# Performance work log

Hardware: AMD Instinct MI355X
Metric: run time of the kernel (lower is better)

Reference implementation:

```python
import jax, jax.numpy as jnp
import numpy as np

N = 32768      # total nodes (2048 graphs * 16 nodes)
E = 491520     # total edges (2048 graphs * 16*15)
F = 11         # in_node_nf
H = 64         # hidden_nf
G = 2048       # number of graphs
NN = 16        # nodes per graph
R = 1024       # n_reactions
L = 4          # n_layers
EIN = 2 * H + 1        # edge_mlp input: [h[row], h[col], radial]
NIN = H + H + F        # node_mlp input: [h, agg, node_attr=h0]


def setup_inputs() -> dict:
    key = jax.random.key(0)
    ks = jax.random.split(key, 24)
    s = 0.05
    d = {
        "h0": jax.random.normal(ks[0], (N, F), jnp.float32),
        "positions": jax.random.normal(ks[1], (N, 3), jnp.float32),
        "edges": jax.random.randint(ks[2], (2, E), 0, N),
        "node_mask": jnp.ones((N, 1), jnp.float32),
        "edge_mask": jnp.ones((E, 1), jnp.float32),
        "reaction_indexes": jax.random.randint(ks[3], (G,), 0, R),
        "reaction_signs": jax.random.normal(ks[4], (G,), jnp.float32),
        # params
        "emb_w": jax.random.normal(ks[5], (F, H), jnp.float32) * s,
        "emb_b": jnp.zeros((H,), jnp.float32),
        "edge_w1": jax.random.normal(ks[6], (L, EIN, H), jnp.float32) * s,
        "edge_b1": jnp.zeros((L, H), jnp.float32),
        "edge_w2": jax.random.normal(ks[7], (L, H, H), jnp.float32) * s,
        "edge_b2": jnp.zeros((L, H), jnp.float32),
        "node_w1": jax.random.normal(ks[8], (L, NIN, H), jnp.float32) * s,
        "node_b1": jnp.zeros((L, H), jnp.float32),
        "node_w2": jax.random.normal(ks[9], (L, H, H), jnp.float32) * s,
        "node_b2": jnp.zeros((L, H), jnp.float32),
        "dec_w1": jax.random.normal(ks[10], (H, H), jnp.float32) * s,
        "dec_b1": jnp.zeros((H,), jnp.float32),
        "dec_w2": jax.random.normal(ks[11], (H, H), jnp.float32) * s,
        "dec_b2": jnp.zeros((H,), jnp.float32),
        "g_w1": jax.random.normal(ks[12], (H, H), jnp.float32) * s,
        "g_b1": jnp.zeros((H,), jnp.float32),
        "g_w2": jax.random.normal(ks[13], (H, 1), jnp.float32) * s,
        "g_b2": jnp.zeros((1,), jnp.float32),
        "n_nodes": NN,
        "n_reactions": R,
    }
    return d


def reference(h0, positions, edges, node_mask, edge_mask, reaction_indexes,
              reaction_signs, emb_w, emb_b, edge_w1, edge_b1, edge_w2, edge_b2,
              node_w1, node_b1, node_w2, node_b2, dec_w1, dec_b1, dec_w2,
              dec_b2, g_w1, g_b1, g_w2, g_b2, n_nodes, n_reactions):
    silu = jax.nn.silu
    row, col = edges[0], edges[1]
    n = h0.shape[0]

    # radial is constant across layers (coords never updated in this variant)
    coord_diff = positions[row] - positions[col]          # [E, 3]
    radial = jnp.sum(coord_diff ** 2, axis=1, keepdims=True)  # [E, 1]

    h = h0 @ emb_w + emb_b                                # [N, H]
    for i in range(edge_w1.shape[0]):
        # edge model
        e_in = jnp.concatenate([h[row], h[col], radial], axis=1)  # [E, 2H+1]
        e = silu(e_in @ edge_w1[i] + edge_b1[i])
        e = silu(e @ edge_w2[i] + edge_b2[i])             # [E, H]
        e = e * edge_mask
        # scatter-sum aggregation by source node
        agg = jax.ops.segment_sum(e, row, num_segments=n)  # [N, H]
        # node model (node_attr = h0)
        n_in = jnp.concatenate([h, agg, h0], axis=1)      # [N, 2H+F]
        h = silu(n_in @ node_w1[i] + node_b1[i]) @ node_w2[i] + node_b2[i]

    # node decoder
    h = silu(h @ dec_w1 + dec_b1) @ dec_w2 + dec_b2
    h = h * node_mask
    # pool per graph (fixed n_nodes per graph)
    hg = h.reshape(-1, n_nodes, h.shape[-1]).sum(axis=1)  # [G, H]
    # graph decoder
    temp = silu(hg @ g_w1 + g_b1) @ g_w2 + g_b2           # [G, 1]
    # signed per-reaction aggregation
    pred = jnp.zeros((n_reactions,), h.dtype).at[reaction_indexes].add(
        temp[:, 0] * reaction_signs)
    return pred
```

## Files before the change

### kernel.cpp

```cpp
#include <hip/hip_runtime.h>
#include <math.h>
#include <stdint.h>

#define N_NODES 32768
#define N_EDGES 491520
#define F_IN    11
#define H       64
#define G_GRAPHS 2048
#define NN_PER_G 16
#define R_REACT 1024
#define L_LAYERS 4
#define EIN     129
#define NIN     139
#define NPBLK   32

#define WPROJ 0
#define WE2   65536
#define WN1   98304
#define WN2   180224
#define WD1   212992
#define WD2   221184
#define WTOT  229376

typedef __attribute__((ext_vector_type(8))) short short8;
// ... 38 lines not shown

    if (b < 64) {
        int l = b >> 4, f = b & 15;
        int nt = f >> 1, kf = f & 1;
#pragma unroll
        for (int j = 0; j < 8; ++j) {
            int row = (nt >= 4 ? 64 : 0) + kf * 32 + quad * 8 + j;
            unsigned short hi, lo;
            splitbf(ew1[l * EIN * H + row * H + (nt & 3) * 16 + m16], hi, lo);
            h8[j] = (short)hi; l8[j] = (short)lo;
        }
        base = wsW + WPROJ + l * 16384; fidx = f; half = 8192;
    } else if (b < 96) {
        int bb = b - 64; int l = bb >> 3, f = bb & 7;
        int nt = f >> 1, kf = f & 1;
#pragma unroll
        for (int j = 0; j < 8; ++j) {
            int row = kf * 32 + quad * 8 + j;
            unsigned short hi, lo;
            splitbf(ew2[l * H * H + row * H + nt * 16 + m16], hi, lo);
            h8[j] = (short)hi; l8[j] = (short)lo;
        }
        base = wsW + WE2 + l * 8192; fidx = f; half = 4096;
    } else if (b < 176) {
        int bb = b - 96; int l = bb / 20, f = bb % 20;
        int nt = f / 5, kf = f % 5;
#pragma unroll
        for (int j = 0; j < 8; ++j) {
            int row = kf * 32 + quad * 8 + j;
            float w = (row < NIN) ? nw1[l * NIN * H + row * H + nt * 16 + m16] : 0.0f;
            unsigned short hi, lo; splitbf(w, hi, lo);
            h8[j] = (short)hi; l8[j] = (short)lo;
        }
        base = wsW + WN1 + l * 20480; fidx = f; half = 10240;
    } else if (b < 208) {
        int bb = b - 176; int l = bb >> 3, f = bb & 7;
        int nt = f >> 1, kf = f & 1;
#pragma unroll
        for (int j = 0; j < 8; ++j) {
            int row = kf * 32 + quad * 8 + j;
            unsigned short hi, lo;
            splitbf(nw2[l * H * H + row * H + nt * 16 + m16], hi, lo);
            h8[j] = (short)hi; l8[j] = (short)lo;
        }
        base = wsW + WN2 + l * 8192; fidx = f; half = 4096;
    } else if (b < 216) {
        int f = b - 208;
        int nt = f >> 1, kf = f & 1;
#pragma unroll
        for (int j = 0; j < 8; ++j) {
            int row = kf * 32 + quad * 8 + j;
            unsigned short hi, lo;
            splitbf(dw1[row * H + nt * 16 + m16], hi, lo);
            h8[j] = (short)hi; l8[j] = (short)lo;
        }
        base = wsW + WD1; fidx = f; half = 4096;
    } else {
        int f = b - 216;
        int nt = f >> 1, kf = f & 1;
#pragma unroll
        for (int j = 0; j < 8; ++j) {
            int row = kf * 32 + quad * 8 + j;
            unsigned short hi, lo;
            splitbf(dw2[row * H + nt * 16 + m16], hi, lo);
            h8[j] = (short)hi; l8[j] = (short)lo;
        }
        base = wsW + WD2; fidx = f; half = 4096;
    }
    *(short8*)(base + (fidx * 64 + lane) * 8) = h8;
    *(short8*)(base + half + (fidx * 64 + lane) * 8) = l8;
}

__global__ __launch_bounds__(256) void k_embed(
        const float* __restrict__ h0, const float* __restrict__ emb_w,
        const float* __restrict__ emb_b, float* __restrict__ h) {
    int tid = blockIdx.x * 256 + threadIdx.x;
    int n = tid >> 6, j = tid & 63;
    float acc = emb_b[j];
#pragma unroll
    for (int k = 0; k < F_IN; ++k)
        acc += h0[n * F_IN + k] * emb_w[k * H + j];
    h[tid] = acc;
}

__global__ __launch_bounds__(256) void k_radial(
        const int* __restrict__ edges, const float* __restrict__ pos,
        float* __restrict__ radial) {
    int e = blockIdx.x * 256 + threadIdx.x;
    int r = edges[e], c = edges[N_EDGES + e];
    float dx = pos[r * 3 + 0] - pos[c * 3 + 0];
    float dy = pos[r * 3 + 1] - pos[c * 3 + 1];
    float dz = pos[r * 3 + 2] - pos[c * 3 + 2];
    radial[e] = dx * dx + dy * dy + dz * dz;
}

__global__ __launch_bounds__(256) void k_hist(
        const int* __restrict__ edges, int* __restrict__ deg) {
    int e = blockIdx.x * 256 + threadIdx.x;
    atomicAdd(&deg[edges[e]], 1);
}

__global__ __launch_bounds__(128) void k_scan_blk(
        const int* __restrict__ deg, int* __restrict__ off,
        int* __restrict__ bsum) {
    __shared__ int sd[128];
    int b = blockIdx.x;
    sd[threadIdx.x] = deg[b * 128 + threadIdx.x];
    __syncthreads();
    if (threadIdx.x == 0) {
        int s = 0;
        for (int i = 0; i < 128; ++i) { int d = sd[i]; sd[i] = s; s += d; }
        bsum[b] = s;
    }
    __syncthreads();
    off[b * 128 + threadIdx.x] = sd[threadIdx.x];
}

__global__ __launch_bounds__(256) void k_scan_top(
        const int* __restrict__ bsum, int* __restrict__ bbase) {
    __shared__ int sb[256];
    sb[threadIdx.x] = bsum[threadIdx.x];
    __syncthreads();
    if (threadIdx.x == 0) {
        int s = 0;
        for (int i = 0; i < 256; ++i) { int d = sb[i]; sb[i] = s; s += d; }
    }
    __syncthreads();
    bbase[threadIdx.x] = sb[threadIdx.x];
}

__global__ __launch_bounds__(256) void k_cursor(
        const int* __restrict__ off, const int* __restrict__ bbase,
        int* __restrict__ nstart, int* __restrict__ cursor) {
    int n = blockIdx.x * 256 + threadIdx.x;
    int ns = off[n] + bbase[n >> 7];
    nstart[n] = ns;
    cursor[n] = ns;
    if (n == 0) nstart[N_NODES] = N_EDGES;
}

__global__ __launch_bounds__(256) void k_fill(
        const int* __restrict__ edges, const float* __restrict__ radial,
        const float* __restrict__ emask, int* __restrict__ cursor,
        int* __restrict__ csrP, float* __restrict__ csrR,
        float* __restrict__ csrM) {
    int e = blockIdx.x * 256 + threadIdx.x;
    int r = edges[e];
    int pos = atomicAdd(&cursor[r], 1);
    csrP[pos] = edges[N_EDGES + e] | ((r & (NPBLK - 1)) << 16);
    csrR[pos] = radial[e];
    csrM[pos] = emask[e];
}

__global__ __launch_bounds__(64, 1) void k_nodeproj_m(
        const float* __restrict__ h, const short* __restrict__ wP,
        const float* __restrict__ b1,
        float* __restrict__ PA, float* __restrict__ PB) {
    const int lane = threadIdx.x;
    const int quad = lane >> 4, m16 = lane & 15;

    short8 Bh[16], Bl[16];
#pragma unroll
    for (int f = 0; f < 16; ++f) {
        Bh[f] = *(const short8*)(wP + (f * 64 + lane) * 8);
        Bl[f] = *(const short8*)(wP + 8192 + (f * 64 + lane) * 8);
    }
    float b1v[4];
#pragma unroll
    for (int nt = 0; nt < 4; ++nt) b1v[nt] = b1[nt * 16 + m16];

    for (int t = 0; t < 2; ++t) {
        const int nb = (blockIdx.x * 2 + t) * 16;
        const float* hp = h + (nb + m16) * H + quad * 8;
        float av[16];
        *(float4*)&av[0]  = *(const float4*)(hp + 0);
        *(float4*)&av[4]  = *(const float4*)(hp + 4);
        *(float4*)&av[8]  = *(const float4*)(hp + 32);
        *(float4*)&av[12] = *(const float4*)(hp + 36);
        short8 Ah0, Ah1, Al0, Al1;
#pragma unroll
        for (int j = 0; j < 8; ++j) {
            unsigned short hi, lo;
            splitbf_t(av[j], hi, lo);     Ah0[j] = (short)hi; Al0[j] = (short)lo;
            splitbf_t(av[8 + j], hi, lo); Ah1[j] = (short)hi; Al1[j] = (short)lo;
        }
        f32x4 acc[8];
#pragma unroll
        for (int nt = 0; nt < 8; ++nt) {
            f32x4 a = {0.0f, 0.0f, 0.0f, 0.0f};
            a = __builtin_amdgcn_mfma_f32_16x16x32_bf16(Ah0, Bh[nt*2+0], a, 0, 0, 0);
            a = __builtin_amdgcn_mfma_f32_16x16x32_bf16(Ah1, Bh[nt*2+1], a, 0, 0, 0);
            a = __builtin_amdgcn_mfma_f32_16x16x32_bf16(Ah0, Bl[nt*2+0], a, 0, 0, 0);
            a = __builtin_amdgcn_mfma_f32_16x16x32_bf16(Ah1, Bl[nt*2+1], a, 0, 0, 0);
            a = __builtin_amdgcn_mfma_f32_16x16x32_bf16(Al0, Bh[nt*2+0], a, 0, 0, 0);
            a = __builtin_amdgcn_mfma_f32_16x16x32_bf16(Al1, Bh[nt*2+1], a, 0, 0, 0);
            acc[nt] = a;
        }
#pragma unroll
        for (int r4 = 0; r4 < 4; ++r4) {
            const int node = nb + quad * 4 + r4;
#pragma unroll
            for (int nt = 0; nt < 4; ++nt)
                PA[node * H + nt * 16 + m16] = acc[nt][r4] + b1v[nt];
#pragma unroll
            for (int nt = 4; nt < 8; ++nt)
                PB[node * H + (nt - 4) * 16 + m16] = acc[nt][r4];
        }
    }
}

__global__ __launch_bounds__(256, 2) void k_edge6(
        const float* __restrict__ PA, const float* __restrict__ PB,
        const int* __restrict__ nstart, const int* __restrict__ csrP,
        const float* __restrict__ csrR, const float* __restrict__ csrM,
        const float* __restrict__ W1,
        const short* __restrict__ wE2, const float* __restrict__ b2,
        float* __restrict__ agg) {
    const int tid = threadIdx.x;
    const int lane = tid & 63, wave = tid >> 6;
    const int quad = lane >> 4, m16 = lane & 15;
    const int n0 = blockIdx.x * NPBLK;

    __shared__ float aggld[NPBLK * 68];
    __shared__ short blds[8 * 64 * 8];
    for (int i = tid; i < NPBLK * 68; i += 256) aggld[i] = 0.0f;
    for (int i = tid; i < 8 * 64; i += 256)
        *(short8*)(blds + i * 8) = *(const short8*)(wE2 + 4096 + i * 8);

    short8 Bh[8];
#pragma unroll
    for (int f = 0; f < 8; ++f)
        Bh[f] = *(const short8*)(wE2 + (f * 64 + lane) * 8);
    float w1cr[16];
#pragma unroll
    for (int i = 0; i < 16; ++i) {
        int k = (i < 8) ? (quad * 8 + i) : (32 + quad * 8 + (i - 8));
        w1cr[i] = W1[128 * H + k];
    }
    float b2v[4];
#pragma unroll
    for (int nt = 0; nt < 4; ++nt) b2v[nt] = b2[nt * 16 + m16];

    const int start = nstart[n0];
    const int end   = nstart[n0 + NPBLK];
    __syncthreads();

    const int ntiles = (end - start + 15) >> 4;

    int   pkA = 0, pkB = 0;
    float radA = 0.0f, radB = 0.0f, mkA = 0.0f, mkB = 0.0f;
    float avA[16], bvA[16];

    int tA = wave;
    bool haveA = tA < ntiles;
    if (haveA) {
        const int idx = start + tA * 16 + m16;
        const int ss  = min(idx, N_EDGES - 1);
        pkA  = csrP[ss];
        radA = csrR[ss];
        mkA  = (idx < end) ? csrM[ss] : 0.0f;
        const int c  = pkA & 0xFFFF;
        const int rl = pkA >> 16;
        const float* par = PA + (n0 + rl) * H + quad * 8;
        const float* pbr = PB + c * H + quad * 8;
        *(float4*)&avA[0]  = *(const float4*)(par + 0);
        *(float4*)&avA[4]  = *(const float4*)(par + 4);
        *(float4*)&avA[8]  = *(const float4*)(par + 32);
        *(float4*)&avA[12] = *(const float4*)(par + 36);
        *(float4*)&bvA[0]  = *(const float4*)(pbr + 0);
        *(float4*)&bvA[4]  = *(const float4*)(pbr + 4);
        *(float4*)&bvA[8]  = *(const float4*)(pbr + 32);
        *(float4*)&bvA[12] = *(const float4*)(pbr + 36);
    }
    int tB = tA + 4;
    bool haveB = tB < ntiles;
    if (haveB) {
        const int idx = start + tB * 16 + m16;
        const int ss  = min(idx, N_EDGES - 1);
        pkB  = csrP[ss];
        radB = csrR[ss];
        mkB  = (idx < end) ? csrM[ss] : 0.0f;
    }

    while (haveA) {
        float bvB[16];
        if (haveB) {
            const int c = pkB & 0xFFFF;
            const float* pbr = PB + c * H + quad * 8;
            *(float4*)&bvB[0]  = *(const float4*)(pbr + 0);
            *(float4*)&bvB[4]  = *(const float4*)(pbr + 4);
            *(float4*)&bvB[8]  = *(const float4*)(pbr + 32);
            *(float4*)&bvB[12] = *(const float4*)(pbr + 36);
        }
        const int tC = tB + 4;
        const bool haveC = tC < ntiles;
        int pkC = 0; float radC = 0.0f, mkC = 0.0f;
        if (haveC) {
            const int idx = start + tC * 16 + m16;
            const int ss  = min(idx, N_EDGES - 1);
            pkC  = csrP[ss];
            radC = csrR[ss];
            mkC  = (idx < end) ? csrM[ss] : 0.0f;
        }

        short8 Ah0, Ah1, Al0, Al1;
#pragma unroll
        for (int i = 0; i < 8; ++i) {
            unsigned short hi, lo;
            splitbf_t(silu_f(avA[i] + bvA[i] + radA * w1cr[i]), hi, lo);
            Ah0[i] = (short)hi; Al0[i] = (short)lo;
            splitbf_t(silu_f(avA[8+i] + bvA[8+i] + radA * w1cr[8+i]), hi, lo);
            Ah1[i] = (short)hi; Al1[i] = (short)lo;
        }
        f32x4 acc[4];
#pragma unroll
        for (int nt = 0; nt < 4; ++nt) {
            f32x4 a = {0.0f, 0.0f, 0.0f, 0.0f};
            a = __builtin_amdgcn_mfma_f32_16x16x32_bf16(Ah0, Bh[nt*2+0], a, 0, 0, 0);
            a = __builtin_amdgcn_mfma_f32_16x16x32_bf16(Ah1, Bh[nt*2+1], a, 0, 0, 0);
            short8 bl0 = *(const short8*)(blds + ((nt*2+0) * 64 + lane) * 8);
            short8 bl1 = *(const short8*)(blds + ((nt*2+1) * 64 + lane) * 8);
            a = __builtin_amdgcn_mfma_f32_16x16x32_bf16(Ah0, bl0, a, 0, 0, 0);
            a = __builtin_amdgcn_mfma_f32_16x16x32_bf16(Ah1, bl1, a, 0, 0, 0);
            a = __builtin_amdgcn_mfma_f32_16x16x32_bf16(Al0, Bh[nt*2+0], a, 0, 0, 0);
            a = __builtin_amdgcn_mfma_f32_16x16x32_bf16(Al1, Bh[nt*2+1], a, 0, 0, 0);
            acc[nt] = a;
        }

        int rlq[4]; float mkq[4];
#pragma unroll
        for (int r4 = 0; r4 < 4; ++r4) {
            rlq[r4] = __shfl(pkA, quad * 4 + r4) >> 16;
            mkq[r4] = __shfl(mkA, quad * 4 + r4);
        }
#pragma unroll
        for (int nt = 0; nt < 4; ++nt) {
            float oo[4];
#pragma unroll
            for (int r4 = 0; r4 < 4; ++r4)
                oo[r4] = silu_f(acc[nt][r4] + b2v[nt]) * mkq[r4];
            int cur = rlq[0]; float s = oo[0];
#pragma unroll
            for (int r4 = 1; r4 < 4; ++r4) {
                if (rlq[r4] == cur) { s += oo[r4]; }
                else {
                    atomicAdd(&aggld[cur * 68 + nt * 16 + m16], s);
                    cur = rlq[r4]; s = oo[r4];
                }
            }
            atomicAdd(&aggld[cur * 68 + nt * 16 + m16], s);
        }

        if (haveB) {
            const int rl = pkB >> 16;
            const float* par = PA + (n0 + rl) * H + quad * 8;
            *(float4*)&avA[0]  = *(const float4*)(par + 0);
            *(float4*)&avA[4]  = *(const float4*)(par + 4);
            *(float4*)&avA[8]  = *(const float4*)(par + 32);
            *(float4*)&avA[12] = *(const float4*)(par + 36);
#pragma unroll
            for (int i = 0; i < 16; ++i) bvA[i] = bvB[i];
            pkA = pkB; radA = radB; mkA = mkB;
        }
        pkB = pkC; radB = radC; mkB = mkC;
        tB = tC; haveA = haveB; haveB = haveC;
    }

    __syncthreads();
#pragma unroll
    for (int i = tid; i < NPBLK * 16; i += 256) {
        int n = i >> 4, cb = (i & 15) << 2;
        *(float4*)&agg[(n0 + n) * H + cb] = *(const float4*)&aggld[n * 68 + cb];
    }
}

__global__ __launch_bounds__(64, 1) void k_node_m(
        float* __restrict__ h, const float* __restrict__ agg,
        const float* __restrict__ h0,
        const short* __restrict__ wN1, const float* __restrict__ b1,
        const short* __restrict__ wN2, const float* __restrict__ b2) {
    const int lane = threadIdx.x;
    const int quad = lane >> 4, m16 = lane & 15;

    short8 B1h[20], B1l[20];
#pragma unroll
    for (int f = 0; f < 20; ++f) {
        B1h[f] = *(const short8*)(wN1 + (f * 64 + lane) * 8);
        B1l[f] = *(const short8*)(wN1 + 10240 + (f * 64 + lane) * 8);
    }
    short8 B2h[8], B2l[8];
#pragma unroll
    for (int f = 0; f < 8; ++f) {
        B2h[f] = *(const short8*)(wN2 + (f * 64 + lane) * 8);
        B2l[f] = *(const short8*)(wN2 + 4096 + (f * 64 + lane) * 8);
    }
    float b1v[4], b2v[4];
#pragma unroll
    for (int nt = 0; nt < 4; ++nt) {
        b1v[nt] = b1[nt * 16 + m16];
        b2v[nt] = b2[nt * 16 + m16];
    }

    __shared__ float tld[16 * 68];

    for (int t = 0; t < 2; ++t) {
        const int nb = (blockIdx.x * 2 + t) * 16;
        float a1[5][8];
        const float* hp = h + (nb + m16) * H + quad * 8;
        const float* ap = agg + (nb + m16) * H + quad * 8;
        *(float4*)&a1[0][0] = *(const float4*)(hp + 0);
        *(float4*)&a1[0][4] = *(const float4*)(hp + 4);
        *(float4*)&a1[1][0] = *(const float4*)(hp + 32);
        *(float4*)&a1[1][4] = *(const float4*)(hp + 36);
        *(float4*)&a1[2][0] = *(const float4*)(ap + 0);
        *(float4*)&a1[2][4] = *(const float4*)(ap + 4);
        *(float4*)&a1[3][0] = *(const float4*)(ap + 32);
        *(float4*)&a1[3][4] = *(const float4*)(ap + 36);
        const float* h0p = h0 + (nb + m16) * F_IN;
#pragma unroll
        for (int j = 0; j < 8; ++j) {
            int kk = quad * 8 + j;
            a1[4][j] = (kk < F_IN) ? h0p[kk] : 0.0f;
        }
        short8 A1h[5], A1l[5];
#pragma unroll
        for (int kf = 0; kf < 5; ++kf) {
            short8 ah, al;
#pragma unroll
            for (int j = 0; j < 8; ++j) {
                unsigned short hi, lo; splitbf_t(a1[kf][j], hi, lo);
                ah[j] = (short)hi; al[j] = (short)lo;
            }
            A1h[kf] = ah; A1l[kf] = al;
        }
        f32x4 acc[4];
#pragma unroll
        for (int nt = 0; nt < 4; ++nt) {
            f32x4 a = {0.0f, 0.0f, 0.0f, 0.0f};
#pragma unroll
            for (int kf = 0; kf < 5; ++kf)
                a = __builtin_amdgcn_mfma_f32_16x16x32_bf16(A1h[kf], B1h[nt*5+kf], a, 0, 0, 0);
#pragma unroll
            for (int kf = 0; kf < 5; ++kf)
                a = __builtin_amdgcn_mfma_f32_16x16x32_bf16(A1h[kf], B1l[nt*5+kf], a, 0, 0, 0);
#pragma unroll
            for (int kf = 0; kf < 5; ++kf)
                a = __builtin_amdgcn_mfma_f32_16x16x32_bf16(A1l[kf], B1h[nt*5+kf], a, 0, 0, 0);
            acc[nt] = a;
        }
#pragma unroll
        for (int r4 = 0; r4 < 4; ++r4)
#pragma unroll
            for (int nt = 0; nt < 4; ++nt)
                tld[(quad * 4 + r4) * 68 + nt * 16 + m16] =
                    silu_f(acc[nt][r4] + b1v[nt]);
        __syncthreads();
        float a2[16];
        *(float4*)&a2[0]  = *(const float4*)&tld[m16 * 68 + quad * 8 + 0];
        *(float4*)&a2[4]  = *(const float4*)&tld[m16 * 68 + quad * 8 + 4];
        *(float4*)&a2[8]  = *(const float4*)&tld[m16 * 68 + quad * 8 + 32];
        *(float4*)&a2[12] = *(const float4*)&tld[m16 * 68 + quad * 8 + 36];
        short8 A2h0, A2h1, A2l0, A2l1;
#pragma unroll
        for (int j = 0; j < 8; ++j) {
            unsigned short hi, lo;
            splitbf_t(a2[j], hi, lo);     A2h0[j] = (short)hi; A2l0[j] = (short)lo;
            splitbf_t(a2[8+j], hi, lo);   A2h1[j] = (short)hi; A2l1[j] = (short)lo;
        }
        f32x4 acc2[4];
#pragma unroll
        for (int nt = 0; nt < 4; ++nt) {
            f32x4 a = {0.0f, 0.0f, 0.0f, 0.0f};
            a = __builtin_amdgcn_mfma_f32_16x16x32_bf16(A2h0, B2h[nt*2+0], a, 0, 0, 0);
            a = __builtin_amdgcn_mfma_f32_16x16x32_bf16(A2h1, B2h[nt*2+1], a, 0, 0, 0);
            a = __builtin_amdgcn_mfma_f32_16x16x32_bf16(A2h0, B2l[nt*2+0], a, 0, 0, 0);
            a = __builtin_amdgcn_mfma_f32_16x16x32_bf16(A2h1, B2l[nt*2+1], a, 0, 0, 0);
            a = __builtin_amdgcn_mfma_f32_16x16x32_bf16(A2l0, B2h[nt*2+0], a, 0, 0, 0);
            a = __builtin_amdgcn_mfma_f32_16x16x32_bf16(A2l1, B2h[nt*2+1], a, 0, 0, 0);
            acc2[nt] = a;
        }
#pragma unroll
        for (int r4 = 0; r4 < 4; ++r4) {
            const int node = nb + quad * 4 + r4;
#pragma unroll
            for (int nt = 0; nt < 4; ++nt)
                h[node * H + nt * 16 + m16] = acc2[nt][r4] + b2v[nt];
        }
        __syncthreads();
    }
}

__global__ __launch_bounds__(64, 1) void k_dec_m(
        float* __restrict__ h, const float* __restrict__ nmask,
        const short* __restrict__ wD1, const float* __restrict__ b1,
        const short* __restrict__ wD2, const float* __restrict__ b2) {
    const int lane = threadIdx.x;
    const int quad = lane >> 4, m16 = lane & 15;

    short8 B1h[8], B1l[8], B2h[8], B2l[8];
#pragma unroll
    for (int f = 0; f < 8; ++f) {
        B1h[f] = *(const short8*)(wD1 + (f * 64 + lane) * 8);
        B1l[f] = *(const short8*)(wD1 + 4096 + (f * 64 + lane) * 8);
        B2h[f] = *(const short8*)(wD2 + (f * 64 + lane) * 8);
        B2l[f] = *(const short8*)(wD2 + 4096 + (f * 64 + lane) * 8);
    }
    float b1v[4], b2v[4];
#pragma unroll
    for (int nt = 0; nt < 4; ++nt) {
        b1v[nt] = b1[nt * 16 + m16];
        b2v[nt] = b2[nt * 16 + m16];
    }
    __shared__ float tld[16 * 68];

    for (int t = 0; t < 2; ++t) {
        const int nb = (blockIdx.x * 2 + t) * 16;
        const float* hp = h + (nb + m16) * H + quad * 8;
        float av[16];
        *(float4*)&av[0]  = *(const float4*)(hp + 0);
        *(float4*)&av[4]  = *(const float4*)(hp + 4);
        *(float4*)&av[8]  = *(const float4*)(hp + 32);
        *(float4*)&av[12] = *(const float4*)(hp + 36);
        short8 Ah0, Ah1, Al0, Al1;
#pragma unroll
        for (int j = 0; j < 8; ++j) {
            unsigned short hi, lo;
            splitbf_t(av[j], hi, lo);     Ah0[j] = (short)hi; Al0[j] = (short)lo;
            splitbf_t(av[8+j], hi, lo);   Ah1[j] = (short)hi; Al1[j] = (short)lo;
        }
        f32x4 acc[4];
#pragma unroll
        for (int nt = 0; nt < 4; ++nt) {
            f32x4 a = {0.0f, 0.0f, 0.0f, 0.0f};
            a = __builtin_amdgcn_mfma_f32_16x16x32_bf16(Ah0, B1h[nt*2+0], a, 0, 0, 0);
            a = __builtin_amdgcn_mfma_f32_16x16x32_bf16(Ah1, B1h[nt*2+1], a, 0, 0, 0);
            a = __builtin_amdgcn_mfma_f32_16x16x32_bf16(Ah0, B1l[nt*2+0], a, 0, 0, 0);
            a = __builtin_amdgcn_mfma_f32_16x16x32_bf16(Ah1, B1l[nt*2+1], a, 0, 0, 0);
            a = __builtin_amdgcn_mfma_f32_16x16x32_bf16(Al0, B1h[nt*2+0], a, 0, 0, 0);
            a = __builtin_amdgcn_mfma_f32_16x16x32_bf16(Al1, B1h[nt*2+1], a, 0, 0, 0);
            acc[nt] = a;
        }
#pragma unroll
        for (int r4 = 0; r4 < 4; ++r4)
#pragma unroll
            for (int nt = 0; nt < 4; ++nt)
                tld[(quad * 4 + r4) * 68 + nt * 16 + m16] =
                    silu_f(acc[nt][r4] + b1v[nt]);
        __syncthreads();
        float a2[16];
        *(float4*)&a2[0]  = *(const float4*)&tld[m16 * 68 + quad * 8 + 0];
        *(float4*)&a2[4]  = *(const float4*)&tld[m16 * 68 + quad * 8 + 4];
        *(float4*)&a2[8]  = *(const float4*)&tld[m16 * 68 + quad * 8 + 32];
        *(float4*)&a2[12] = *(const float4*)&tld[m16 * 68 + quad * 8 + 36];
        short8 A2h0, A2h1, A2l0, A2l1;
#pragma unroll
        for (int j = 0; j < 8; ++j) {
            unsigned short hi, lo;
            splitbf_t(a2[j], hi, lo);     A2h0[j] = (short)hi; A2l0[j] = (short)lo;
            splitbf_t(a2[8+j], hi, lo);   A2h1[j] = (short)hi; A2l1[j] = (short)lo;
        }
        f32x4 acc2[4];
#pragma unroll
        for (int nt = 0; nt < 4; ++nt) {
            f32x4 a = {0.0f, 0.0f, 0.0f, 0.0f};
            a = __builtin_amdgcn_mfma_f32_16x16x32_bf16(A2h0, B2h[nt*2+0], a, 0, 0, 0);
            a = __builtin_amdgcn_mfma_f32_16x16x32_bf16(A2h1, B2h[nt*2+1], a, 0, 0, 0);
            a = __builtin_amdgcn_mfma_f32_16x16x32_bf16(A2h0, B2l[nt*2+0], a, 0, 0, 0);
            a = __builtin_amdgcn_mfma_f32_16x16x32_bf16(A2h1, B2l[nt*2+1], a, 0, 0, 0);
            a = __builtin_amdgcn_mfma_f32_16x16x32_bf16(A2l0, B2h[nt*2+0], a, 0, 0, 0);
            a = __builtin_amdgcn_mfma_f32_16x16x32_bf16(A2l1, B2h[nt*2+1], a, 0, 0, 0);
            acc2[nt] = a;
        }
#pragma unroll
        for (int r4 = 0; r4 < 4; ++r4) {
            const int node = nb + quad * 4 + r4;
            const float nm = nmask[node];
#pragma unroll
            for (int nt = 0; nt < 4; ++nt)
                h[node * H + nt * 16 + m16] = (acc2[nt][r4] + b2v[nt]) * nm;
        }
        __syncthreads();
    }
}

__global__ __launch_bounds__(64) void k_graph(
        const float* __restrict__ h, const int* __restrict__ rid,
        const float* __restrict__ rsign,
        const float* __restrict__ W1, const float* __restrict__ b1,
        const float* __restrict__ W2, const float* __restrict__ b2,
        float* __restrict__ pred) {
    const int g = blockIdx.x;
    const int lane = threadIdx.x;
    float hgv = 0.0f;
#pragma unroll
    for (int m = 0; m < NN_PER_G; ++m)
        hgv += h[(g * NN_PER_G + m) * H + lane];
    __shared__ __align__(16) float hgs[64];
    hgs[lane] = hgv;
    __syncthreads();
    float acc = b1[lane];
#pragma unroll
    for (int k = 0; k < H; ++k)
        acc += hgs[k] * W1[k * H + lane];
    float part = silu_f(acc) * W2[lane];
#pragma unroll
    for (int off = 32; off > 0; off >>= 1)
        part += __shfl_down(part, off);
    if (lane == 0)
        atomAddF(&pred[rid[g]], (part + b2[0]) * rsign[g]);
}

extern "C" void kernel_launch(void* const* d_in, const int* in_sizes, int n_in,
                              void* d_out, int out_size, void* d_ws, size_t ws_size,
                              hipStream_t stream) {
    const float* h0      = (const float*)d_in[0];
    const float* pos     = (const float*)d_in[1];
    const int*   edges   = (const int*)d_in[2];
    const float* nmask   = (const float*)d_in[3];
    const float* emask   = (const float*)d_in[4];
    const int*   rid     = (const int*)d_in[5];
    const float* rsign   = (const float*)d_in[6];
    const float* emb_w   = (const float*)d_in[7];
    const float* emb_b   = (const float*)d_in[8];
    const float* edge_w1 = (const float*)d_in[9];
    const float* edge_b1 = (const float*)d_in[10];
    const float* edge_w2 = (const float*)d_in[11];
    const float* edge_b2 = (const float*)d_in[12];
    const float* node_w1 = (const float*)d_in[13];
    const float* node_b1 = (const float*)d_in[14];
    const float* node_w2 = (const float*)d_in[15];
    const float* node_b2 = (const float*)d_in[16];
    const float* dec_w1  = (const float*)d_in[17];
    const float* dec_b1  = (const float*)d_in[18];
    const float* dec_w2  = (const float*)d_in[19];
    const float* dec_b2  = (const float*)d_in[20];
    const float* g_w1    = (const float*)d_in[21];
    const float* g_b1    = (const float*)d_in[22];
    const float* g_w2    = (const float*)d_in[23];
    const float* g_b2    = (const float*)d_in[24];

    float* h      = (float*)d_ws;
    float* agg    = h + N_NODES * H;
    float* radial = agg + N_NODES * H;
    float* PA     = radial + N_EDGES;
    float* PB     = PA + N_NODES * H;
    float* csrR   = PB + N_NODES * H;
    float* csrM   = csrR + N_EDGES;
    int*   csrP   = (int*)(csrM + N_EDGES);
    int*   deg    = csrP + N_EDGES;
    int*   off    = deg + N_NODES;
    int*   bsum   = off + N_NODES;
    int*   bbase  = bsum + 256;
    int*   nstart = bbase + 256;
    int*   cursor = nstart + N_NODES + 1;
    short* wsW    = (short*)((((uintptr_t)(cursor + N_NODES)) + 255) & ~(uintptr_t)255);
    float* pred   = (float*)d_out;

    hipMemsetAsync(d_out, 0, R_REACT * sizeof(float), stream);
    hipMemsetAsync(deg, 0, N_NODES * sizeof(int), stream);

    k_prepw<<<224, 64, 0, stream>>>(edge_w1, edge_w2, node_w1, node_w2,
                                    dec_w1, dec_w2, wsW);
    k_embed<<<(N_NODES * H) / 256, 256, 0, stream>>>(h0, emb_w, emb_b, h);
    k_radial<<<N_EDGES / 256, 256, 0, stream>>>(edges, pos, radial);
    k_hist<<<N_EDGES / 256, 256, 0, stream>>>(edges, deg);
    k_scan_blk<<<256, 128, 0, stream>>>(deg, off, bsum);
    k_scan_top<<<1, 256, 0, stream>>>(bsum, bbase);
    k_cursor<<<N_NODES / 256, 256, 0, stream>>>(off, bbase, nstart, cursor);
    k_fill<<<N_EDGES / 256, 256, 0, stream>>>(edges, radial, emask, cursor,
                                              csrP, csrR, csrM);

    for (int i = 0; i < L_LAYERS; ++i) {
        k_nodeproj_m<<<N_NODES / 32, 64, 0, stream>>>(
            h, wsW + WPROJ + i * 16384, edge_b1 + i * H, PA, PB);
        k_edge6<<<N_NODES / NPBLK, 256, 0, stream>>>(
            PA, PB, nstart, csrP, csrR, csrM,
            edge_w1 + i * EIN * H,
            wsW + WE2 + i * 8192, edge_b2 + i * H, agg);
        k_node_m<<<N_NODES / 32, 64, 0, stream>>>(
            h, agg, h0,
            wsW + WN1 + i * 20480, node_b1 + i * H,
            wsW + WN2 + i * 8192,  node_b2 + i * H);
    }
    k_dec_m<<<N_NODES / 32, 64, 0, stream>>>(h, nmask, wsW + WD1, dec_b1,
                                             wsW + WD2, dec_b2);
    k_graph<<<G_GRAPHS, 64, 0, stream>>>(h, rid, rsign, g_w1, g_b1, g_w2,
                                         g_b2, pred);
}
```

Measured before the change: 563.6 us.

## Stream weights per tile in node kernels and hold edge weights in registers

The node projection, node MLP and decoder kernels stop preloading every weight fragment into registers. They now handle one 16-node tile per block, reload the weights inside the output-column loop, and launch twice as many blocks with a higher occupancy hint. The edge kernel moves the low-half second-layer weights from LDS into registers. It also reads the row-local index and mask per quad straight from the CSR arrays instead of using shuffles, and it fixes the tA tile rotation. Register pressure and block size go down in exchange for more repeated global or L2 weight loads, and the edge kernel uses more registers.

```diff
diff --git a/kernel.cpp b/kernel.cpp
--- a/kernel.cpp
+++ b/kernel.cpp
@@ -214,59 +214,51 @@
     csrM[pos] = emask[e];
 }
 
-__global__ __launch_bounds__(64, 1) void k_nodeproj_m(
+__global__ __launch_bounds__(64, 2) void k_nodeproj_m(
         const float* __restrict__ h, const short* __restrict__ wP,
         const float* __restrict__ b1,
         float* __restrict__ PA, float* __restrict__ PB) {
     const int lane = threadIdx.x;
     const int quad = lane >> 4, m16 = lane & 15;
-
-    short8 Bh[16], Bl[16];
-#pragma unroll
-    for (int f = 0; f < 16; ++f) {
-        Bh[f] = *(const short8*)(wP + (f * 64 + lane) * 8);
-        Bl[f] = *(const short8*)(wP + 8192 + (f * 64 + lane) * 8);
-    }
+    const int nb = blockIdx.x * 16;
+
+    const float* hp = h + (nb + m16) * H + quad * 8;
+    float av[16];
+    *(float4*)&av[0]  = *(const float4*)(hp + 0);
+    *(float4*)&av[4]  = *(const float4*)(hp + 4);
+    *(float4*)&av[8]  = *(const float4*)(hp + 32);
+    *(float4*)&av[12] = *(const float4*)(hp + 36);
     float b1v[4];
 #pragma unroll
     for (int nt = 0; nt < 4; ++nt) b1v[nt] = b1[nt * 16 + m16];
 
-    for (int t = 0; t < 2; ++t) {
-        const int nb = (blockIdx.x * 2 + t) * 16;
-        const float* hp = h + (nb + m16) * H + quad * 8;
-        float av[16];
-        *(float4*)&av[0]  = *(const float4*)(hp + 0);
-        *(float4*)&av[4]  = *(const float4*)(hp + 4);
-        *(float4*)&av[8]  = *(const float4*)(hp + 32);
-        *(float4*)&av[12] = *(const float4*)(hp + 36);
-        short8 Ah0, Ah1, Al0, Al1;
-#pragma unroll
-        for (int j = 0; j < 8; ++j) {
-            unsigned short hi, lo;
-            splitbf_t(av[j], hi, lo);     Ah0[j] = (short)hi; Al0[j] = (short)lo;
-            splitbf_t(av[8 + j], hi, lo); Ah1[j] = (short)hi; Al1[j] = (short)lo;
-        }
-        f32x4 acc[8];
-#pragma unroll
-        for (int nt = 0; nt < 8; ++nt) {
-            f32x4 a = {0.0f, 0.0f, 0.0f, 0.0f};
-            a = __builtin_amdgcn_mfma_f32_16x16x32_bf16(Ah0, Bh[nt*2+0], a, 0, 0, 0);
-            a = __builtin_amdgcn_mfma_f32_16x16x32_bf16(Ah1, Bh[nt*2+1], a, 0, 0, 0);
-            a = __builtin_amdgcn_mfma_f32_16x16x32_bf16(Ah0, Bl[nt*2+0], a, 0, 0, 0);
-            a = __builtin_amdgcn_mfma_f32_16x16x32_bf16(Ah1, Bl[nt*2+1], a, 0, 0, 0);
-            a = __builtin_amdgcn_mfma_f32_16x16x32_bf16(Al0, Bh[nt*2+0], a, 0, 0, 0);
-            a = __builtin_amdgcn_mfma_f32_16x16x32_bf16(Al1, Bh[nt*2+1], a, 0, 0, 0);
-            acc[nt] = a;
-        }
+    short8 Ah0, Ah1, Al0, Al1;
+#pragma unroll
+    for (int j = 0; j < 8; ++j) {
+        unsigned short hi, lo;
+        splitbf_t(av[j], hi, lo);     Ah0[j] = (short)hi; Al0[j] = (short)lo;
+        splitbf_t(av[8 + j], hi, lo); Ah1[j] = (short)hi; Al1[j] = (short)lo;
+    }
+#pragma unroll
+    for (int nt = 0; nt < 8; ++nt) {
+        short8 bh0 = *(const short8*)(wP + ((nt*2+0) * 64 + lane) * 8);
+        short8 bh1 = *(const short8*)(wP + ((nt*2+1) * 64 + lane) * 8);
+        short8 bl0 = *(const short8*)(wP + 8192 + ((nt*2+0) * 64 + lane) * 8);
+        short8 bl1 = *(const short8*)(wP + 8192 + ((nt*2+1) * 64 + lane) * 8);
+        f32x4 a = {0.0f, 0.0f, 0.0f, 0.0f};
+        a = __builtin_amdgcn_mfma_f32_16x16x32_bf16(Ah0, bh0, a, 0, 0, 0);
+        a = __builtin_amdgcn_mfma_f32_16x16x32_bf16(Ah1, bh1, a, 0, 0, 0);
+        a = __builtin_amdgcn_mfma_f32_16x16x32_bf16(Ah0, bl0, a, 0, 0, 0);
+        a = __builtin_amdgcn_mfma_f32_16x16x32_bf16(Ah1, bl1, a, 0, 0, 0);
+        a = __builtin_amdgcn_mfma_f32_16x16x32_bf16(Al0, bh0, a, 0, 0, 0);
+        a = __builtin_amdgcn_mfma_f32_16x16x32_bf16(Al1, bh1, a, 0, 0, 0);
 #pragma unroll
         for (int r4 = 0; r4 < 4; ++r4) {
             const int node = nb + quad * 4 + r4;
-#pragma unroll
-            for (int nt = 0; nt < 4; ++nt)
-                PA[node * H + nt * 16 + m16] = acc[nt][r4] + b1v[nt];
-#pragma unroll
-            for (int nt = 4; nt < 8; ++nt)
-                PB[node * H + (nt - 4) * 16 + m16] = acc[nt][r4];
+            if (nt < 4)
+                PA[node * H + nt * 16 + m16] = a[r4] + b1v[nt];
+            else
+                PB[node * H + (nt - 4) * 16 + m16] = a[r4];
         }
     }
 }
@@ -284,15 +276,14 @@
     const int n0 = blockIdx.x * NPBLK;
 
     __shared__ float aggld[NPBLK * 68];
-    __shared__ short blds[8 * 64 * 8];
     for (int i = tid; i < NPBLK * 68; i += 256) aggld[i] = 0.0f;
-    for (int i = tid; i < 8 * 64; i += 256)
-        *(short8*)(blds + i * 8) = *(const short8*)(wE2 + 4096 + i * 8);
-
-    short8 Bh[8];
-#pragma unroll
-    for (int f = 0; f < 8; ++f)
+
+    short8 Bh[8], Bl[8];
+#pragma unroll
+    for (int f = 0; f < 8; ++f) {
         Bh[f] = *(const short8*)(wE2 + (f * 64 + lane) * 8);
+        Bl[f] = *(const short8*)(wE2 + 4096 + (f * 64 + lane) * 8);
+    }
     float w1cr[16];
 #pragma unroll
     for (int i = 0; i < 16; ++i) {
@@ -310,7 +301,7 @@
     const int ntiles = (end - start + 15) >> 4;
 
     int   pkA = 0, pkB = 0;
-    float radA = 0.0f, radB = 0.0f, mkA = 0.0f, mkB = 0.0f;
+    float radA = 0.0f, radB = 0.0f;
     float avA[16], bvA[16];
 
     int tA = wave;
@@ -320,7 +311,6 @@
         const int ss  = min(idx, N_EDGES - 1);
         pkA  = csrP[ss];
         radA = csrR[ss];
-        mkA  = (idx < end) ? csrM[ss] : 0.0f;
         const int c  = pkA & 0xFFFF;
         const int rl = pkA >> 16;
         const float* par = PA + (n0 + rl) * H + quad * 8;
@@ -341,7 +331,6 @@
         const int ss  = min(idx, N_EDGES - 1);
         pkB  = csrP[ss];
         radB = csrR[ss];
-        mkB  = (idx < end) ? csrM[ss] : 0.0f;
     }
 
     while (haveA) {
@@ -356,13 +345,20 @@
         }
         const int tC = tB + 4;
         const bool haveC = tC < ntiles;
-        int pkC = 0; float radC = 0.0f, mkC = 0.0f;
+        int pkC = 0; float radC = 0.0f;
         if (haveC) {
             const int idx = start + tC * 16 + m16;
             const int ss  = min(idx, N_EDGES - 1);
             pkC  = csrP[ss];
             radC = csrR[ss];
-            mkC  = (idx < end) ? csrM[ss] : 0.0f;
+        }
+        int rlq[4]; float mkq[4];
+        const int sb = start + tA * 16 + quad * 4;
+#pragma unroll
+        for (int r4 = 0; r4 < 4; ++r4) {
+            int s = sb + r4, s2 = min(s, N_EDGES - 1);
+            rlq[r4] = csrP[s2] >> 16;
+            mkq[r4] = (s < end) ? csrM[s2] : 0.0f;
         }
 
         short8 Ah0, Ah1, Al0, Al1;
@@ -380,21 +376,13 @@
             f32x4 a = {0.0f, 0.0f, 0.0f, 0.0f};
             a = __builtin_amdgcn_mfma_f32_16x16x32_bf16(Ah0, Bh[nt*2+0], a, 0, 0, 0);
             a = __builtin_amdgcn_mfma_f32_16x16x32_bf16(Ah1, Bh[nt*2+1], a, 0, 0, 0);
-            short8 bl0 = *(const short8*)(blds + ((nt*2+0) * 64 + lane) * 8);
-            short8 bl1 = *(const short8*)(blds + ((nt*2+1) * 64 + lane) * 8);
-            a = __builtin_amdgcn_mfma_f32_16x16x32_bf16(Ah0, bl0, a, 0, 0, 0);
-            a = __builtin_amdgcn_mfma_f32_16x16x32_bf16(Ah1, bl1, a, 0, 0, 0);
+            a = __builtin_amdgcn_mfma_f32_16x16x32_bf16(Ah0, Bl[nt*2+0], a, 0, 0, 0);
+            a = __builtin_amdgcn_mfma_f32_16x16x32_bf16(Ah1, Bl[nt*2+1], a, 0, 0, 0);
             a = __builtin_amdgcn_mfma_f32_16x16x32_bf16(Al0, Bh[nt*2+0], a, 0, 0, 0);
             a = __builtin_amdgcn_mfma_f32_16x16x32_bf16(Al1, Bh[nt*2+1], a, 0, 0, 0);
             acc[nt] = a;
         }
 
-        int rlq[4]; float mkq[4];
-#pragma unroll
-        for (int r4 = 0; r4 < 4; ++r4) {
-            rlq[r4] = __shfl(pkA, quad * 4 + r4) >> 16;
-            mkq[r4] = __shfl(mkA, quad * 4 + r4);
-        }
 #pragma unroll
         for (int nt = 0; nt < 4; ++nt) {
             float oo[4];
@@ -422,10 +410,10 @@
             *(float4*)&avA[12] = *(const float4*)(par + 36);
 #pragma unroll
             for (int i = 0; i < 16; ++i) bvA[i] = bvB[i];
-            pkA = pkB; radA = radB; mkA = mkB;
-        }
-        pkB = pkC; radB = radC; mkB = mkC;
-        tB = tC; haveA = haveB; haveB = haveC;
+            pkA = pkB; radA = radB;
+        }
+        pkB = pkC; radB = radC;
+        tA = tB; tB = tC; haveA = haveB; haveB = haveC;
     }
 
     __syncthreads();
@@ -436,26 +424,15 @@
     }
 }
 
-__global__ __launch_bounds__(64, 1) void k_node_m(
+__global__ __launch_bounds__(64, 2) void k_node_m(
         float* __restrict__ h, const float* __restrict__ agg,
         const float* __restrict__ h0,
         const short* __restrict__ wN1, const float* __restrict__ b1,
         const short* __restrict__ wN2, const float* __restrict__ b2) {
     const int lane = threadIdx.x;
     const int quad = lane >> 4, m16 = lane & 15;
-
-    short8 B1h[20], B1l[20];
-#pragma unroll
-    for (int f = 0; f < 20; ++f) {
-        B1h[f] = *(const short8*)(wN1 + (f * 64 + lane) * 8);
-        B1l[f] = *(const short8*)(wN1 + 10240 + (f * 64 + lane) * 8);
-    }
-    short8 B2h[8], B2l[8];
-#pragma unroll
-    for (int f = 0; f < 8; ++f) {
-        B2h[f] = *(const short8*)(wN2 + (f * 64 + lane) * 8);
-        B2l[f] = *(const short8*)(wN2 + 4096 + (f * 64 + lane) * 8);
-    }
+    const int nb = blockIdx.x * 16;
+
     float b1v[4], b2v[4];
 #pragma unroll
     for (int nt = 0; nt < 4; ++nt) {
@@ -465,108 +442,98 @@
 
     __shared__ float tld[16 * 68];
 
-    for (int t = 0; t < 2; ++t) {
-        const int nb = (blockIdx.x * 2 + t) * 16;
-        float a1[5][8];
-        const float* hp = h + (nb + m16) * H + quad * 8;
-        const float* ap = agg + (nb + m16) * H + quad * 8;
-        *(float4*)&a1[0][0] = *(const float4*)(hp + 0);
-        *(float4*)&a1[0][4] = *(const float4*)(hp + 4);
-        *(float4*)&a1[1][0] = *(const float4*)(hp + 32);
-        *(float4*)&a1[1][4] = *(const float4*)(hp + 36);
-        *(float4*)&a1[2][0] = *(const float4*)(ap + 0);
-        *(float4*)&a1[2][4] = *(const float4*)(ap + 4);
-        *(float4*)&a1[3][0] = *(const float4*)(ap + 32);
-        *(float4*)&a1[3][4] = *(const float4*)(ap + 36);
-        const float* h0p = h0 + (nb + m16) * F_IN;
+    float a1[5][8];
+    const float* hp = h + (nb + m16) * H + quad * 8;
+    const float* ap = agg + (nb + m16) * H + quad * 8;
+    *(float4*)&a1[0][0] = *(const float4*)(hp + 0);
+    *(float4*)&a1[0][4] = *(const float4*)(hp + 4);
+    *(float4*)&a1[1][0] = *(const float4*)(hp + 32);
+    *(float4*)&a1[1][4] = *(const float4*)(hp + 36);
+    *(float4*)&a1[2][0] = *(const float4*)(ap + 0);
+    *(float4*)&a1[2][4] = *(const float4*)(ap + 4);
+    *(float4*)&a1[3][0] = *(const float4*)(ap + 32);
+    *(float4*)&a1[3][4] = *(const float4*)(ap + 36);
+    const float* h0p = h0 + (nb + m16) * F_IN;
+#pragma unroll
+    for (int j = 0; j < 8; ++j) {
+        int kk = quad * 8 + j;
+        a1[4][j] = (kk < F_IN) ? h0p[kk] : 0.0f;
+    }
+    short8 A1h[5], A1l[5];
+#pragma unroll
+    for (int kf = 0; kf < 5; ++kf) {
+        short8 ah, al;
 #pragma unroll
         for (int j = 0; j < 8; ++j) {
-            int kk = quad * 8 + j;
-            a1[4][j] = (kk < F_IN) ? h0p[kk] : 0.0f;
-        }
-        short8 A1h[5], A1l[5];
+            unsigned short hi, lo; splitbf_t(a1[kf][j], hi, lo);
+            ah[j] = (short)hi; al[j] = (short)lo;
+        }
+        A1h[kf] = ah; A1l[kf] = al;
+    }
+#pragma unroll
+    for (int nt = 0; nt < 4; ++nt) {
+        short8 bh[5], bl[5];
 #pragma unroll
         for (int kf = 0; kf < 5; ++kf) {
-            short8 ah, al;
-#pragma unroll
-            for (int j = 0; j < 8; ++j) {
-                unsigned short hi, lo; splitbf_t(a1[kf][j], hi, lo);
-                ah[j] = (short)hi; al[j] = (short)lo;
-            }
-            A1h[kf] = ah; A1l[kf] = al;
-        }
-        f32x4 acc[4];
-#pragma unroll
-        for (int nt = 0; nt < 4; ++nt) {
-            f32x4 a = {0.0f, 0.0f, 0.0f, 0.0f};
-#pragma unroll
-            for (int kf = 0; kf < 5; ++kf)
-                a = __builtin_amdgcn_mfma_f32_16x16x32_bf16(A1h[kf], B1h[nt*5+kf], a, 0, 0, 0);
-#pragma unroll
-            for (int kf = 0; kf < 5; ++kf)
-                a = __builtin_amdgcn_mfma_f32_16x16x32_bf16(A1h[kf], B1l[nt*5+kf], a, 0, 0, 0);
-#pragma unroll
-            for (int kf = 0; kf < 5; ++kf)
-                a = __builtin_amdgcn_mfma_f32_16x16x32_bf16(A1l[kf], B1h[nt*5+kf], a, 0, 0, 0);
-            acc[nt] = a;
-        }
+            bh[kf] = *(const short8*)(wN1 + ((nt*5+kf) * 64 + lane) * 8);
+            bl[kf] = *(const short8*)(wN1 + 10240 + ((nt*5+kf) * 64 + lane) * 8);
+        }
+        f32x4 a = {0.0f, 0.0f, 0.0f, 0.0f};
+#pragma unroll
+        for (int kf = 0; kf < 5; ++kf)
+            a = __builtin_amdgcn_mfma_f32_16x16x32_bf16(A1h[kf], bh[kf], a, 0, 0, 0);
+#pragma unroll
+        for (int kf = 0; kf < 5; ++kf)
+            a = __builtin_amdgcn_mfma_f32_16x16x32_bf16(A1h[kf], bl[kf], a, 0, 0, 0);
+#pragma unroll
+        for (int kf = 0; kf < 5; ++kf)
+            a = __builtin_amdgcn_mfma_f32_16x16x32_bf16(A1l[kf], bh[kf], a, 0, 0, 0);
 #pragma unroll
         for (int r4 = 0; r4 < 4; ++r4)
-#pragma unroll
-            for (int nt = 0; nt < 4; ++nt)
-                tld[(quad * 4 + r4) * 68 + nt * 16 + m16] =
-                    silu_f(acc[nt][r4] + b1v[nt]);
-        __syncthreads();
-        float a2[16];
-        *(float4*)&a2[0]  = *(const float4*)&tld[m16 * 68 + quad * 8 + 0];
-        *(float4*)&a2[4]  = *(const float4*)&tld[m16 * 68 + quad * 8 + 4];
-        *(float4*)&a2[8]  = *(const float4*)&tld[m16 * 68 + quad * 8 + 32];
-        *(float4*)&a2[12] = *(const float4*)&tld[m16 * 68 + quad * 8 + 36];
-        short8 A2h0, A2h1, A2l0, A2l1;
-#pragma unroll
-        for (int j = 0; j < 8; ++j) {
-            unsigned short hi, lo;
-            splitbf_t(a2[j], hi, lo);     A2h0[j] = (short)hi; A2l0[j] = (short)lo;
-            splitbf_t(a2[8+j], hi, lo);   A2h1[j] = (short)hi; A2l1[j] = (short)lo;
-        }
-        f32x4 acc2[4];
-#pragma unroll
-        for (int nt = 0; nt < 4; ++nt) {
-            f32x4 a = {0.0f, 0.0f, 0.0f, 0.0f};
-            a = __builtin_amdgcn_mfma_f32_16x16x32_bf16(A2h0, B2h[nt*2+0], a, 0, 0, 0);
-            a = __builtin_amdgcn_mfma_f32_16x16x32_bf16(A2h1, B2h[nt*2+1], a, 0, 0, 0);
-            a = __builtin_amdgcn_mfma_f32_16x16x32_bf16(A2h0, B2l[nt*2+0], a, 0, 0, 0);
-            a = __builtin_amdgcn_mfma_f32_16x16x32_bf16(A2h1, B2l[nt*2+1], a, 0, 0, 0);
-            a = __builtin_amdgcn_mfma_f32_16x16x32_bf16(A2l0, B2h[nt*2+0], a, 0, 0, 0);
-            a = __builtin_amdgcn_mfma_f32_16x16x32_bf16(A2l1, B2h[nt*2+1], a, 0, 0, 0);
-            acc2[nt] = a;
-        }
+            tld[(quad * 4 + r4) * 68 + nt * 16 + m16] = silu_f(a[r4] + b1v[nt]);
+    }
+    __syncthreads();
+    float a2[16];
+    *(float4*)&a2[0]  = *(const float4*)&tld[m16 * 68 + quad * 8 + 0];
+    *(float4*)&a2[4]  = *(const float4*)&tld[m16 * 68 + quad * 8 + 4];
+    *(float4*)&a2[8]  = *(const float4*)&tld[m16 * 68 + quad * 8 + 32];
+    *(float4*)&a2[12] = *(const float4*)&tld[m16 * 68 + quad * 8 + 36];
+    short8 A2h0, A2h1, A2l0, A2l1;
+#pragma unroll
+    for (int j = 0; j < 8; ++j) {
+        unsigned short hi, lo;
+        splitbf_t(a2[j], hi, lo);     A2h0[j] = (short)hi; A2l0[j] = (short)lo;
+        splitbf_t(a2[8+j], hi, lo);   A2h1[j] = (short)hi; A2l1[j] = (short)lo;
+    }
+#pragma unroll
+    for (int nt = 0; nt < 4; ++nt) {
+        short8 bh0 = *(const short8*)(wN2 + ((nt*2+0) * 64 + lane) * 8);
+        short8 bh1 = *(const short8*)(wN2 + ((nt*2+1) * 64 + lane) * 8);
+        short8 bl0 = *(const short8*)(wN2 + 4096 + ((nt*2+0) * 64 + lane) * 8);
+        short8 bl1 = *(const short8*)(wN2 + 4096 + ((nt*2+1) * 64 + lane) * 8);
+        f32x4 a = {0.0f, 0.0f, 0.0f, 0.0f};
+        a = __builtin_amdgcn_mfma_f32_16x16x32_bf16(A2h0, bh0, a, 0, 0, 0);
+        a = __builtin_amdgcn_mfma_f32_16x16x32_bf16(A2h1, bh1, a, 0, 0, 0);
+        a = __builtin_amdgcn_mfma_f32_16x16x32_bf16(A2h0, bl0, a, 0, 0, 0);
+        a = __builtin_amdgcn_mfma_f32_16x16x32_bf16(A2h1, bl1, a, 0, 0, 0);
+        a = __builtin_amdgcn_mfma_f32_16x16x32_bf16(A2l0, bh0, a, 0, 0, 0);
+        a = __builtin_amdgcn_mfma_f32_16x16x32_bf16(A2l1, bh1, a, 0, 0, 0);
 #pragma unroll
         for (int r4 = 0; r4 < 4; ++r4) {
             const int node = nb + quad * 4 + r4;
-#pragma unroll
-            for (int nt = 0; nt < 4; ++nt)
-                h[node * H + nt * 16 + m16] = acc2[nt][r4] + b2v[nt];
-        }
-        __syncthreads();
-    }
-}
-
-__global__ __launch_bounds__(64, 1) void k_dec_m(
+            h[node * H + nt * 16 + m16] = a[r4] + b2v[nt];
+        }
+    }
+}
+
+__global__ __launch_bounds__(64, 2) void k_dec_m(
         float* __restrict__ h, const float* __restrict__ nmask,
         const short* __restrict__ wD1, const float* __restrict__ b1,
         const short* __restrict__ wD2, const float* __restrict__ b2) {
     const int lane = threadIdx.x;
     const int quad = lane >> 4, m16 = lane & 15;
-
-    short8 B1h[8], B1l[8], B2h[8], B2l[8];
-#pragma unroll
-    for (int f = 0; f < 8; ++f) {
-        B1h[f] = *(const short8*)(wD1 + (f * 64 + lane) * 8);
-        B1l[f] = *(const short8*)(wD1 + 4096 + (f * 64 + lane) * 8);
-        B2h[f] = *(const short8*)(wD2 + (f * 64 + lane) * 8);
-        B2l[f] = *(const short8*)(wD2 + 4096 + (f * 64 + lane) * 8);
-    }
+    const int nb = blockIdx.x * 16;
+
     float b1v[4], b2v[4];
 #pragma unroll
     for (int nt = 0; nt < 4; ++nt) {
@@ -575,73 +542,68 @@
     }
     __shared__ float tld[16 * 68];
 
-    for (int t = 0; t < 2; ++t) {
-        const int nb = (blockIdx.x * 2 + t) * 16;
-        const float* hp = h + (nb + m16) * H + quad * 8;
-        float av[16];
-        *(float4*)&av[0]  = *(const float4*)(hp + 0);
-        *(float4*)&av[4]  = *(const float4*)(hp + 4);
-        *(float4*)&av[8]  = *(const float4*)(hp + 32);
-        *(float4*)&av[12] = *(const float4*)(hp + 36);
-        short8 Ah0, Ah1, Al0, Al1;
-#pragma unroll
-        for (int j = 0; j < 8; ++j) {
-            unsigned short hi, lo;
-            splitbf_t(av[j], hi, lo);     Ah0[j] = (short)hi; Al0[j] = (short)lo;
-            splitbf_t(av[8+j], hi, lo);   Ah1[j] = (short)hi; Al1[j] = (short)lo;
-        }
-        f32x4 acc[4];
-#pragma unroll
-        for (int nt = 0; nt < 4; ++nt) {
-            f32x4 a = {0.0f, 0.0f, 0.0f, 0.0f};
-            a = __builtin_amdgcn_mfma_f32_16x16x32_bf16(Ah0, B1h[nt*2+0], a, 0, 0, 0);
-            a = __builtin_amdgcn_mfma_f32_16x16x32_bf16(Ah1, B1h[nt*2+1], a, 0, 0, 0);
-            a = __builtin_amdgcn_mfma_f32_16x16x32_bf16(Ah0, B1l[nt*2+0], a, 0, 0, 0);
-            a = __builtin_amdgcn_mfma_f32_16x16x32_bf16(Ah1, B1l[nt*2+1], a, 0, 0, 0);
-            a = __builtin_amdgcn_mfma_f32_16x16x32_bf16(Al0, B1h[nt*2+0], a, 0, 0, 0);
-            a = __builtin_amdgcn_mfma_f32_16x16x32_bf16(Al1, B1h[nt*2+1], a, 0, 0, 0);
-            acc[nt] = a;
-        }
+    const float* hp = h + (nb + m16) * H + quad * 8;
+    float av[16];
+    *(float4*)&av[0]  = *(const float4*)(hp + 0);
+    *(float4*)&av[4]  = *(const float4*)(hp + 4);
+    *(float4*)&av[8]  = *(const float4*)(hp + 32);
+    *(float4*)&av[12] = *(const float4*)(hp + 36);
+    short8 Ah0, Ah1, Al0, Al1;
+#pragma unroll
+    for (int j = 0; j < 8; ++j) {
+        unsigned short hi, lo;
+        splitbf_t(av[j], hi, lo);     Ah0[j] = (short)hi; Al0[j] = (short)lo;
+        splitbf_t(av[8+j], hi, lo);   Ah1[j] = (short)hi; Al1[j] = (short)lo;
+    }
+#pragma unroll
+    for (int nt = 0; nt < 4; ++nt) {
+        short8 bh0 = *(const short8*)(wD1 + ((nt*2+0) * 64 + lane) * 8);
+        short8 bh1 = *(const short8*)(wD1 + ((nt*2+1) * 64 + lane) * 8);
+        short8 bl0 = *(const short8*)(wD1 + 4096 + ((nt*2+0) * 64 + lane) * 8);
+        short8 bl1 = *(const short8*)(wD1 + 4096 + ((nt*2+1) * 64 + lane) * 8);
+        f32x4 a = {0.0f, 0.0f, 0.0f, 0.0f};
+        a = __builtin_amdgcn_mfma_f32_16x16x32_bf16(Ah0, bh0, a, 0, 0, 0);
+        a = __builtin_amdgcn_mfma_f32_16x16x32_bf16(Ah1, bh1, a, 0, 0, 0);
+        a = __builtin_amdgcn_mfma_f32_16x16x32_bf16(Ah0, bl0, a, 0, 0, 0);
+        a = __builtin_amdgcn_mfma_f32_16x16x32_bf16(Ah1, bl1, a, 0, 0, 0);
+        a = __builtin_amdgcn_mfma_f32_16x16x32_bf16(Al0, bh0, a, 0, 0, 0);
+        a = __builtin_amdgcn_mfma_f32_16x16x32_bf16(Al1, bh1, a, 0, 0, 0);
 #pragma unroll
         for (int r4 = 0; r4 < 4; ++r4)
-#pragma unroll
-            for (int nt = 0; nt < 4; ++nt)
-                tld[(quad * 4 + r4) * 68 + nt * 16 + m16] =
-                    silu_f(acc[nt][r4] + b1v[nt]);
-        __syncthreads();
-        float a2[16];
-        *(float4*)&a2[0]  = *(const float4*)&tld[m16 * 68 + quad * 8 + 0];
-        *(float4*)&a2[4]  = *(const float4*)&tld[m16 * 68 + quad * 8 + 4];
-        *(float4*)&a2[8]  = *(const float4*)&tld[m16 * 68 + quad * 8 + 32];
-        *(float4*)&a2[12] = *(const float4*)&tld[m16 * 68 + quad * 8 + 36];
-        short8 A2h0, A2h1, A2l0, A2l1;
-#pragma unroll
-        for (int j = 0; j < 8; ++j) {
-            unsigned short hi, lo;
-            splitbf_t(a2[j], hi, lo);     A2h0[j] = (short)hi; A2l0[j] = (short)lo;
-            splitbf_t(a2[8+j], hi, lo);   A2h1[j] = (short)hi; A2l1[j] = (short)lo;
-        }
-        f32x4 acc2[4];
-#pragma unroll
-        for (int nt = 0; nt < 4; ++nt) {
-            f32x4 a = {0.0f, 0.0f, 0.0f, 0.0f};
-            a = __builtin_amdgcn_mfma_f32_16x16x32_bf16(A2h0, B2h[nt*2+0], a, 0, 0, 0);
-            a = __builtin_amdgcn_mfma_f32_16x16x32_bf16(A2h1, B2h[nt*2+1], a, 0, 0, 0);
-            a = __builtin_amdgcn_mfma_f32_16x16x32_bf16(A2h0, B2l[nt*2+0], a, 0, 0, 0);
-            a = __builtin_amdgcn_mfma_f32_16x16x32_bf16(A2h1, B2l[nt*2+1], a, 0, 0, 0);
-            a = __builtin_amdgcn_mfma_f32_16x16x32_bf16(A2l0, B2h[nt*2+0], a, 0, 0, 0);
-            a = __builtin_amdgcn_mfma_f32_16x16x32_bf16(A2l1, B2h[nt*2+1], a, 0, 0, 0);
-            acc2[nt] = a;
-        }
+            tld[(quad * 4 + r4) * 68 + nt * 16 + m16] = silu_f(a[r4] + b1v[nt]);
+    }
+    __syncthreads();
+    float a2[16];
+    *(float4*)&a2[0]  = *(const float4*)&tld[m16 * 68 + quad * 8 + 0];
+    *(float4*)&a2[4]  = *(const float4*)&tld[m16 * 68 + quad * 8 + 4];
+    *(float4*)&a2[8]  = *(const float4*)&tld[m16 * 68 + quad * 8 + 32];
+    *(float4*)&a2[12] = *(const float4*)&tld[m16 * 68 + quad * 8 + 36];
+    short8 A2h0, A2h1, A2l0, A2l1;
+#pragma unroll
+    for (int j = 0; j < 8; ++j) {
+        unsigned short hi, lo;
+        splitbf_t(a2[j], hi, lo);     A2h0[j] = (short)hi; A2l0[j] = (short)lo;
+        splitbf_t(a2[8+j], hi, lo);   A2h1[j] = (short)hi; A2l1[j] = (short)lo;
+    }
+#pragma unroll
+    for (int nt = 0; nt < 4; ++nt) {
+        short8 bh0 = *(const short8*)(wD2 + ((nt*2+0) * 64 + lane) * 8);
+        short8 bh1 = *(const short8*)(wD2 + ((nt*2+1) * 64 + lane) * 8);
+        short8 bl0 = *(const short8*)(wD2 + 4096 + ((nt*2+0) * 64 + lane) * 8);
+        short8 bl1 = *(const short8*)(wD2 + 4096 + ((nt*2+1) * 64 + lane) * 8);
+        f32x4 a = {0.0f, 0.0f, 0.0f, 0.0f};
+        a = __builtin_amdgcn_mfma_f32_16x16x32_bf16(A2h0, bh0, a, 0, 0, 0);
+        a = __builtin_amdgcn_mfma_f32_16x16x32_bf16(A2h1, bh1, a, 0, 0, 0);
+        a = __builtin_amdgcn_mfma_f32_16x16x32_bf16(A2h0, bl0, a, 0, 0, 0);
+        a = __builtin_amdgcn_mfma_f32_16x16x32_bf16(A2h1, bl1, a, 0, 0, 0);
+        a = __builtin_amdgcn_mfma_f32_16x16x32_bf16(A2l0, bh0, a, 0, 0, 0);
+        a = __builtin_amdgcn_mfma_f32_16x16x32_bf16(A2l1, bh1, a, 0, 0, 0);
 #pragma unroll
         for (int r4 = 0; r4 < 4; ++r4) {
             const int node = nb + quad * 4 + r4;
             const float nm = nmask[node];
-#pragma unroll
-            for (int nt = 0; nt < 4; ++nt)
-                h[node * H + nt * 16 + m16] = (acc2[nt][r4] + b2v[nt]) * nm;
-        }
-        __syncthreads();
+            h[node * H + nt * 16 + m16] = (a[r4] + b2v[nt]) * nm;
+        }
     }
 }
 
@@ -733,18 +695,18 @@
                                               csrP, csrR, csrM);
 
     for (int i = 0; i < L_LAYERS; ++i) {
-        k_nodeproj_m<<<N_NODES / 32, 64, 0, stream>>>(
+        k_nodeproj_m<<<N_NODES / 16, 64, 0, stream>>>(
             h, wsW + WPROJ + i * 16384, edge_b1 + i * H, PA, PB);
         k_edge6<<<N_NODES / NPBLK, 256, 0, stream>>>(
             PA, PB, nstart, csrP, csrR, csrM,
             edge_w1 + i * EIN * H,
             wsW + WE2 + i * 8192, edge_b2 + i * H, agg);
-        k_node_m<<<N_NODES / 32, 64, 0, stream>>>(
+        k_node_m<<<N_NODES / 16, 64, 0, stream>>>(
             h, agg, h0,
             wsW + WN1 + i * 20480, node_b1 + i * H,
             wsW + WN2 + i * 8192,  node_b2 + i * H);
     }
-    k_dec_m<<<N_NODES / 32, 64, 0, stream>>>(h, nmask, wsW + WD1, dec_b1,
+    k_dec_m<<<N_NODES / 16, 64, 0, stream>>>(h, nmask, wsW + WD1, dec_b1,
                                              wsW + WD2, dec_b2);
     k_graph<<<G_GRAPHS, 64, 0, stream>>>(h, rid, rsign, g_w1, g_b1, g_w2,
                                          g_b2, pred);
```

New measurement: 524.9 us. 6.9% less time.
